# Performance work log

Hardware: AMD Instinct MI355X
Metric: run time of the kernel (lower is better)

The kernel has to match this reference:

```python
import jax, jax.numpy as jnp
import numpy as np

HEADS = 16
TOPK = 2048  # dsa_topk


def setup_inputs() -> dict:
    key = jax.random.key(0)
    ks = jax.random.split(key, 9)
    B, Q, KV, C = 2, 2048, 16384, 1024
    w = lambda k: jax.random.normal(k, (C, C), dtype=jnp.float32) * 0.02
    return {
        "hidden_states": jax.random.normal(ks[0], (B, Q, C), dtype=jnp.float32),
        "encoder_hidden_states": jax.random.normal(ks[1], (B, KV, C), dtype=jnp.float32),
        "Wq": w(ks[2]),
        "Wk": w(ks[3]),
        "Wv": w(ks[4]),
        "Wo": w(ks[5]),
        "bo": jnp.zeros((C,), dtype=jnp.float32),
        "Wg": jax.random.normal(ks[6], (C, C), dtype=jnp.float32) * 0.01,  # xavier gain 0.1
        "bg": jnp.full((C,), -1.5, dtype=jnp.float32),  # gate_init_bias
    }


def reference(hidden_states, encoder_hidden_states, Wq, Wk, Wv, Wo, bo, Wg, bg):
    B, Q, C = hidden_states.shape
    H = HEADS
    D = C // H
    scale = 1.0 / jnp.sqrt(jnp.asarray(D, dtype=hidden_states.dtype))

    # projections -> [B, H, S, D]
    q = (hidden_states @ Wq).reshape(B, Q, H, D).transpose(0, 2, 1, 3)
    k = (encoder_hidden_states @ Wk).reshape(B, -1, H, D).transpose(0, 2, 1, 3)
    v = (encoder_hidden_states @ Wv).reshape(B, -1, H, D).transpose(0, 2, 1, 3)

    # _sparse_select: query-summary scored top-k KV gather (kv_len > TOPK here)
    q_summary = q.mean(axis=2)                                   # [B, H, D]
    sel_score = jnp.einsum("bhd,bhkd->bhk", q_summary, k) * scale
    idx = jax.lax.top_k(sel_score, TOPK)[1]                      # [B, H, TOPK]
    k_sel = jnp.take_along_axis(k, idx[..., None], axis=2)       # [B, H, TOPK, D]
    v_sel = jnp.take_along_axis(v, idx[..., None], axis=2)

    # attention over selected KV
    scores = jnp.einsum("bhqd,bhkd->bhqk", q, k_sel) * scale
    probs = jax.nn.softmax(scores.astype(jnp.float32), axis=-1).astype(scores.dtype)
    out = jnp.einsum("bhqk,bhkd->bhqd", probs, v_sel)
    out = out.transpose(0, 2, 1, 3).reshape(B, Q, C)

    # sigmoid gate + output projection (to_out[1] dropout is identity at eval)
    out = out * jax.nn.sigmoid(out @ Wg + bg)
    out = out @ Wo + bo

    # residual_connection=True, rescale_output_factor=1.0
    return out + hidden_states
```

## Files before the change

kernel.cpp:

```cpp
#include <hip/hip_runtime.h>
#include <hip/hip_bf16.h>

typedef unsigned short u16;
typedef __bf16 bf16x8 __attribute__((ext_vector_type(8)));
typedef float f32x4 __attribute__((ext_vector_type(4)));

__device__ __forceinline__ u16 f2bf(float f) {
    union { float f; unsigned int u; } v; v.f = f;
    unsigned int u = v.u;
    unsigned int r = (u + 0x7fffu + ((u >> 16) & 1u)) >> 16;
    return (u16)r;
}
__device__ __forceinline__ float bf2f(u16 b) {
    union { unsigned int u; float f; } v; v.u = ((unsigned int)b) << 16;
    return v.f;
}

__device__ __forceinline__ void glds16(const u16* g, u16* l) {
    __builtin_amdgcn_global_load_lds(
        (__attribute__((address_space(1))) void*)(g),
        (__attribute__((address_space(3))) void*)(l), 16, 0, 0);
}

__global__ __launch_bounds__(256) void cast_bf16_kernel(const float* __restrict__ src,
                                                        u16* __restrict__ dst, int n4) {
    int i = blockIdx.x * 256 + threadIdx.x;
    if (i >= n4) return;
    float4 v = ((const float4*)src)[i];
    ushort4 o;
    o.x = f2bf(v.x); o.y = f2bf(v.y); o.z = f2bf(v.z); o.w = f2bf(v.w);
    ((ushort4*)dst)[i] = o;
}

__global__ __launch_bounds__(256) void transpose_cast_kernel(
    const float* __restrict__ Wq, const float* __restrict__ Wk, const float* __restrict__ Wv,
    const float* __restrict__ Wg, const float* __restrict__ Wo,
    u16* __restrict__ WqT, u16* __restrict__ WkvT, u16* __restrict__ WgT, u16* __restrict__ WoT) {
    __shared__ float tile[32][33];
    const float* src; u16* dst;
    switch (blockIdx.z) {
        case 0: src = Wq; dst = WqT; break;
        case 1: src = Wk; dst = WkvT; break;
        case 2: src = Wv; dst = WkvT + (size_t)1024 * 1024; break;
        case 3: src = Wg; dst = WgT; break;
        default: src = Wo; dst = WoT; break;
    }
    int n0 = blockIdx.x * 32, k0 = blockIdx.y * 32;
    int tx = threadIdx.x, ty = threadIdx.y;
    #pragma unroll
    for (int j = 0; j < 4; j++)
        tile[ty + j * 8][tx] = src[(size_t)(k0 + ty + j * 8) * 1024 + n0 + tx];
    __syncthreads();
    #pragma unroll
    for (int j = 0; j < 4; j++)
        dst[(size_t)(n0 + ty + j * 8) * 1024 + k0 + tx] = f2bf(tile[tx][ty + j * 8]);
}

template <int EPI>
__global__ __launch_bounds__(256) void gemm_bf16(
    const u16* __restrict__ A, const u16* __restrict__ B, int ldc,
    u16* __restrict__ Cbf, const float* __restrict__ bias,
    const u16* __restrict__ mul_src, const float* __restrict__ add_src,
    float* __restrict__ Cf) {
    constexpr int K = 1024;
    const int tid = threadIdx.x;
    const int w = tid >> 6, l = tid & 63;
    const int lr = l & 15, lg = l >> 4;
    const int wr = w >> 1, wc = w & 1;
    const int m0 = blockIdx.y * 128, n0 = blockIdx.x * 128;

    __shared__ u16 As[128 * 64];
    __shared__ u16 Bs[128 * 64];

    const f32x4 fz = {0.f, 0.f, 0.f, 0.f};
    f32x4 acc[4][4];
    #pragma unroll
    for (int i = 0; i < 4; i++)
        #pragma unroll
        for (int j = 0; j < 4; j++) acc[i][j] = fz;

    const int lane_row = l >> 3;
    const int lane_sl  = l & 7;
    const int src_ch   = lane_sl ^ lane_row;
    const u16* Ab = A + (size_t)(m0 + w * 32 + lane_row) * K + src_ch * 8;
    const u16* Bb = B + (size_t)(n0 + w * 32 + lane_row) * K + src_ch * 8;

    for (int kt = 0; kt < K; kt += 64) {
        __syncthreads();
        #pragma unroll
        for (int j = 0; j < 4; j++) {
            glds16(Ab + (size_t)j * 8 * K + kt, As + (w * 32 + j * 8) * 64);
            glds16(Bb + (size_t)j * 8 * K + kt, Bs + (w * 32 + j * 8) * 64);
        }
        __syncthreads();
        #pragma unroll
        for (int kk = 0; kk < 2; kk++) {
            bf16x8 af[4], bfr[4];
            #pragma unroll
            for (int mi = 0; mi < 4; mi++) {
                int row = wr * 64 + mi * 16 + lr;
                int ch = (kk * 4 + lg) ^ (row & 7);
                af[mi] = *(const bf16x8*)(As + row * 64 + ch * 8);
            }
            #pragma unroll
            for (int ni = 0; ni < 4; ni++) {
                int row = wc * 64 + ni * 16 + lr;
                int ch = (kk * 4 + lg) ^ (row & 7);
                bfr[ni] = *(const bf16x8*)(Bs + row * 64 + ch * 8);
            }
            #pragma unroll
            for (int mi = 0; mi < 4; mi++)
                #pragma unroll
                for (int ni = 0; ni < 4; ni++)
                    acc[mi][ni] = __builtin_amdgcn_mfma_f32_16x16x32_bf16(
                        af[mi], bfr[ni], acc[mi][ni], 0, 0, 0);
        }
    }

    #pragma unroll
    for (int mi = 0; mi < 4; mi++) {
        #pragma unroll
        for (int ni = 0; ni < 4; ni++) {
            #pragma unroll
            for (int r = 0; r < 4; r++) {
                int gm = m0 + wr * 64 + mi * 16 + lg * 4 + r;
                int gn = n0 + wc * 64 + ni * 16 + lr;
                float v = acc[mi][ni][r];
                if (EPI == 0) {
                    Cbf[(size_t)gm * ldc + gn] = f2bf(v);
                } else if (EPI == 2) {
                    float g = v + bias[gn];
                    float a = bf2f(mul_src[(size_t)gm * ldc + gn]);
                    float sg = 1.f / (1.f + __expf(-g));
                    Cbf[(size_t)gm * ldc + gn] = f2bf(a * sg);
                } else {
                    Cf[(size_t)gm * ldc + gn] = v + bias[gn] + add_src[(size_t)gm * ldc + gn];
                }
            }
        }
    }
}

__global__ __launch_bounds__(256) void hsum1_kernel(const float* __restrict__ hidden,
                                                    float* __restrict__ part) {
    int b = blockIdx.x, chunk = blockIdx.y;
    int tid = threadIdx.x;
    const float4* src = (const float4*)(hidden + ((size_t)b * 2048 + chunk * 16) * 1024) + tid;
    float4 acc = {0.f, 0.f, 0.f, 0.f};
    #pragma unroll
    for (int r = 0; r < 16; r++) {
        float4 v = src[r * 256];
        acc.x += v.x; acc.y += v.y; acc.z += v.z; acc.w += v.w;
    }
    ((float4*)(part + ((size_t)b * 128 + chunk) * 1024))[tid] = acc;
}

__global__ __launch_bounds__(256) void hsum2_kernel(const float* __restrict__ part,
                                                    float* __restrict__ hm) {
    int b = blockIdx.x, tid = threadIdx.x;
    const float4* src = (const float4*)(part + (size_t)b * 128 * 1024) + tid;
    float4 acc = {0.f, 0.f, 0.f, 0.f};
    for (int c = 0; c < 128; c++) {
        float4 v = src[c * 256];
        acc.x += v.x; acc.y += v.y; acc.z += v.z; acc.w += v.w;
    }
    const float inv = 1.f / 2048.f;
    acc.x *= inv; acc.y *= inv; acc.z *= inv; acc.w *= inv;
    ((float4*)(hm + (size_t)b * 1024))[tid] = acc;
}

__global__ __launch_bounds__(256) void qz_kernel(const float* __restrict__ hm,
                                                 const u16* __restrict__ WqT,
                                                 const u16* __restrict__ WkT,
                                                 u16* __restrict__ z_bf) {
    int bh = blockIdx.x, b = bh >> 4, h = bh & 15;
    int tid = threadIdx.x;
    __shared__ float hm_l[1024];
    __shared__ float qs_l[64];
    __shared__ float red[256];
    ((float4*)hm_l)[tid] = ((const float4*)(hm + (size_t)b * 1024))[tid];
    __syncthreads();
    {
        int d = tid >> 2, q = tid & 3;
        const u16* wq = WqT + (size_t)(h * 64 + d) * 1024 + q * 256;
        float a = 0.f;
        for (int i = 0; i < 256; i += 8) {
            uint4 u = *(const uint4*)(wq + i);
            const u16* p = (const u16*)&u;
            #pragma unroll
            for (int j = 0; j < 8; j++) a += bf2f(p[j]) * hm_l[q * 256 + i + j];
        }
        red[tid] = a;
    }
    __syncthreads();
    if (tid < 64)
        qs_l[tid] = red[tid * 4] + red[tid * 4 + 1] + red[tid * 4 + 2] + red[tid * 4 + 3];
    __syncthreads();
    {
        float z0 = 0.f, z1 = 0.f, z2 = 0.f, z3 = 0.f;
        for (int d = 0; d < 64; d++) {
            float qs = qs_l[d];
            const u16* wk = WkT + (size_t)(h * 64 + d) * 1024 + tid * 4;
            uint2 u = *(const uint2*)wk;
            const u16* p = (const u16*)&u;
            z0 += qs * bf2f(p[0]); z1 += qs * bf2f(p[1]);
            z2 += qs * bf2f(p[2]); z3 += qs * bf2f(p[3]);
        }
        ushort4 o;
        o.x = f2bf(z0); o.y = f2bf(z1); o.z = f2bf(z2); o.w = f2bf(z3);
        *(ushort4*)(z_bf + (size_t)bh * 1024 + tid * 4) = o;
    }
}

__global__ __launch_bounds__(256) void escore_kernel(const float* __restrict__ enc,
                                                     const u16* __restrict__ z_bf,
                                                     u16* __restrict__ ebf,
                                                     float* __restrict__ score) {
    const int b = blockIdx.y, kv0 = blockIdx.x * 64;
    const int tid = threadIdx.x, w = tid >> 6, l = tid & 63;
    const int lr = l & 15, lg = l >> 4;
    __shared__ u16 e_lds[64 * 64];

    const int row2 = tid >> 3;
    const int cgrp = tid & 7;
    const float* ebase = enc + (size_t)(b * 16384 + kv0) * 1024;
    u16* obase = ebf + (size_t)(b * 16384 + kv0) * 1024;
    const u16* zb = z_bf + (size_t)b * 16 * 1024;

    float4 rv[2][2];
    auto loadT = [&](int kt) {
        #pragma unroll
        for (int jj = 0; jj < 2; jj++) {
            int row = row2 + jj * 32;
            rv[jj][0] = *(const float4*)(ebase + (size_t)row * 1024 + kt + cgrp * 8);
            rv[jj][1] = *(const float4*)(ebase + (size_t)row * 1024 + kt + cgrp * 8 + 4);
        }
    };
    loadT(0);

    const f32x4 fz = {0.f, 0.f, 0.f, 0.f};
    f32x4 acc = fz;

    for (int kt = 0; kt < 1024; kt += 64) {
        #pragma unroll
        for (int jj = 0; jj < 2; jj++) {
            int row = row2 + jj * 32;
            union { u16 u[8]; uint4 v; } pk;
            pk.u[0] = f2bf(rv[jj][0].x); pk.u[1] = f2bf(rv[jj][0].y);
            pk.u[2] = f2bf(rv[jj][0].z); pk.u[3] = f2bf(rv[jj][0].w);
            pk.u[4] = f2bf(rv[jj][1].x); pk.u[5] = f2bf(rv[jj][1].y);
            pk.u[6] = f2bf(rv[jj][1].z); pk.u[7] = f2bf(rv[jj][1].w);
            *(uint4*)(e_lds + row * 64 + ((cgrp ^ (row & 7)) * 8)) = pk.v;
            *(uint4*)(obase + (size_t)row * 1024 + kt + cgrp * 8) = pk.v;
        }
        __syncthreads();
        if (kt + 64 < 1024) loadT(kt + 64);
        #pragma unroll
        for (int ks = 0; ks < 2; ks++) {
            bf16x8 af = *(const bf16x8*)(zb + (size_t)lr * 1024 + kt + ks * 32 + lg * 8);
            int brow = w * 16 + lr;
            bf16x8 bf_ = *(const bf16x8*)(e_lds + brow * 64 + (((ks * 4 + lg) ^ (brow & 7))) * 8);
            acc = __builtin_amdgcn_mfma_f32_16x16x32_bf16(af, bf_, acc, 0, 0, 0);
        }
        __syncthreads();
    }
    #pragma unroll
    for (int r = 0; r < 4; r++)
        score[(size_t)(b * 16 + lg * 4 + r) * 16384 + kv0 + w * 16 + lr] = acc[r];
}

__global__ __launch_bounds__(1024) void select_kernel(const float* __restrict__ score,
                                                      int* __restrict__ sel_idx) {
    const int bh = blockIdx.x;
    const float* sc = score + (size_t)bh * 16384;
    const int tid = threadIdx.x;
    const int grp = tid >> 8;

    __shared__ int hist[4][256];
    __shared__ int total[256];
    __shared__ int bc[4];

    u16 key[16];
    #pragma unroll
    for (int j = 0; j < 16; j++) {
        unsigned int b = __float_as_uint(sc[tid + j * 1024]);
        unsigned int ui = (b & 0x80000000u) ? ~b : (b | 0x80000000u);
        key[j] = (u16)(ui >> 16);
    }

    ((int*)hist)[tid] = 0;
    __syncthreads();
    #pragma unroll
    for (int j = 0; j < 16; j++) atomicAdd(&hist[grp][key[j] >> 8], 1);
    __syncthreads();
    if (tid < 256) total[tid] = hist[0][tid] + hist[1][tid] + hist[2][tid] + hist[3][tid];
    __syncthreads();
    if (tid == 0) {
        int want = 2048, acc = 0;
        for (int dd = 255; dd >= 0; dd--) {
            acc += total[dd];
            if (acc >= want) { bc[0] = dd; bc[1] = want - (acc - total[dd]); break; }
        }
    }
    __syncthreads();
    const int hi = bc[0];
    const int want1 = bc[1];

    ((int*)hist)[tid] = 0;
    __syncthreads();
    #pragma unroll
    for (int j = 0; j < 16; j++)
        if ((key[j] >> 8) == hi) atomicAdd(&hist[grp][key[j] & 0xff], 1);
    __syncthreads();
    if (tid < 256) total[tid] = hist[0][tid] + hist[1][tid] + hist[2][tid] + hist[3][tid];
    __syncthreads();
    if (tid == 0) {
        int want = want1, acc = 0;
        for (int dd = 255; dd >= 0; dd--) {
            acc += total[dd];
            if (acc >= want) { bc[0] = (hi << 8) | dd; bc[1] = want - (acc - total[dd]); break; }
        }
        bc[2] = 0; bc[3] = 0;
    }
    __syncthreads();
    const u16 thr = (u16)bc[0];
    const int n_eq = bc[1];
    const int base_eq = 2048 - n_eq;

    int* out = sel_idx + (size_t)bh * 2048;
    #pragma unroll
    for (int j = 0; j < 16; j++) {
        int i = tid + j * 1024;
        if (key[j] > thr) {
            int p = atomicAdd(&bc[2], 1);
            out[p] = i;
        } else if (key[j] == thr) {
            int p = atomicAdd(&bc[3], 1);
            if (p < n_eq) out[base_eq + p] = i;
        }
    }
}

__global__ __launch_bounds__(256) void selproj_kernel(const u16* __restrict__ ebf,
                                                      const u16* __restrict__ WkvT,
                                                      const int* __restrict__ sel_idx,
                                                      u16* __restrict__ k_sel,
                                                      u16* __restrict__ v_selT) {
    const int bh = blockIdx.y, b = bh >> 4, h = bh & 15;
    const int t0 = blockIdx.x * 128;
    const int tid = threadIdx.x, w = tid >> 6, l = tid & 63;
    const int lr = l & 15, lg = l >> 4;
    const int lane_row = l >> 3, src_ch = (l & 7) ^ lane_row;

    __shared__ u16 e_lds[128 * 64];
    __shared__ u16 w_lds[128 * 64];

    int encrow[4], wrow[4];
    #pragma unroll
    for (int j = 0; j < 4; j++) {
        int t = t0 + w * 32 + j * 8 + lane_row;
        encrow[j] = b * 16384 + sel_idx[(size_t)bh * 2048 + t];
        int r = w * 32 + j * 8 + lane_row;
        wrow[j] = (r < 64) ? (h * 64 + r) : (1024 + h * 64 + (r & 63));
    }

    const f32x4 fz = {0.f, 0.f, 0.f, 0.f};
    f32x4 acc_k[2][4], acc_v[8];
    #pragma unroll
    for (int i = 0; i < 2; i++)
        #pragma unroll
        for (int j = 0; j < 4; j++) acc_k[i][j] = fz;
    #pragma unroll
    for (int i = 0; i < 8; i++) acc_v[i] = fz;

    for (int kt = 0; kt < 1024; kt += 64) {
        __syncthreads();
        #pragma unroll
        for (int j = 0; j < 4; j++) {
            glds16(ebf + (size_t)encrow[j] * 1024 + kt + src_ch * 8, e_lds + (w * 32 + j * 8) * 64);
            glds16(WkvT + (size_t)wrow[j] * 1024 + kt + src_ch * 8, w_lds + (w * 32 + j * 8) * 64);
        }
        __syncthreads();
        #pragma unroll
        for (int ks = 0; ks < 2; ks++) {
            bf16x8 ae[2];
            #pragma unroll
            for (int mi = 0; mi < 2; mi++) {
                int row = w * 32 + mi * 16 + lr;
                ae[mi] = *(const bf16x8*)(e_lds + row * 64 + (((ks * 4 + lg) ^ (row & 7))) * 8);
            }
            bf16x8 aw;
            {
                int row = 64 + w * 16 + lr;
                aw = *(const bf16x8*)(w_lds + row * 64 + (((ks * 4 + lg) ^ (row & 7))) * 8);
            }
            #pragma unroll
            for (int ni = 0; ni < 4; ni++) {
                int row = ni * 16 + lr;
                bf16x8 bw = *(const bf16x8*)(w_lds + row * 64 + (((ks * 4 + lg) ^ (row & 7))) * 8);
                acc_k[0][ni] = __builtin_amdgcn_mfma_f32_16x16x32_bf16(ae[0], bw, acc_k[0][ni], 0, 0, 0);
                acc_k[1][ni] = __builtin_amdgcn_mfma_f32_16x16x32_bf16(ae[1], bw, acc_k[1][ni], 0, 0, 0);
            }
            #pragma unroll
            for (int ni = 0; ni < 8; ni++) {
                int row = ni * 16 + lr;
                bf16x8 be = *(const bf16x8*)(e_lds + row * 64 + (((ks * 4 + lg) ^ (row & 7))) * 8);
                acc_v[ni] = __builtin_amdgcn_mfma_f32_16x16x32_bf16(aw, be, acc_v[ni], 0, 0, 0);
            }
        }
    }

    u16* kb = k_sel + (size_t)bh * 2048 * 64;
    #pragma unroll
    for (int mi = 0; mi < 2; mi++)
        #pragma unroll
        for (int ni = 0; ni < 4; ni++)
            #pragma unroll
            for (int r = 0; r < 4; r++) {
                int t = t0 + w * 32 + mi * 16 + lg * 4 + r;
                int d = ni * 16 + lr;
                kb[(size_t)t * 64 + (((d >> 3) ^ (t & 7)) * 8) + (d & 7)] = f2bf(acc_k[mi][ni][r]);
            }
    u16* vb = v_selT + (size_t)bh * 64 * 2048;
    #pragma unroll
    for (int ni = 0; ni < 8; ni++)
        #pragma unroll
        for (int r = 0; r < 4; r++) {
            int d = w * 16 + lg * 4 + r;
            int t = t0 + ni * 16 + lr;
            int tl = t & 63;
            int kap = (tl & 15) * 4 + (tl >> 4);
            vb[(size_t)d * 2048 + (t & ~63) + (((kap >> 3) ^ (d & 7)) * 8) + (kap & 7)] =
                f2bf(acc_v[ni][r]);
        }
}

__global__ __launch_bounds__(512) void attn_kernel(
    const u16* __restrict__ q_bf, const u16* __restrict__ k_sel,
    const u16* __restrict__ v_selT, u16* __restrict__ attn_out) {
    const int bh = blockIdx.y, b = bh >> 4, h = bh & 15;
    const int q0 = blockIdx.x * 128;
    const int tid = threadIdx.x, w = tid >> 6, l = tid & 63;
    const int lr = l & 15, lg = l >> 4;
    const int lk = lr & 7;
    const float SC = 0.18033688011f;
    const float THR = 11.0f;

    __shared__ u16 k_lds[2][64 * 64];
    __shared__ u16 vt_lds[64 * 64];
    __shared__ u16 p_lds[8][16][68];

    const u16* qb = q_bf + ((size_t)b * 2048 + q0 + w * 16 + lr) * 1024 + h * 64;
    bf16x8 qf0 = *(const bf16x8*)(qb + lg * 8);
    bf16x8 qf1 = *(const bf16x8*)(qb + 32 + lg * 8);

    const f32x4 fz = {0.f, 0.f, 0.f, 0.f};
    f32x4 o[4];
    #pragma unroll
    for (int f = 0; f < 4; f++) o[f] = fz;
    float mm = -1e30f;
    float l_part[4] = {0.f, 0.f, 0.f, 0.f};

    const u16* kb  = k_sel + (size_t)bh * 2048 * 64;
    const u16* vtb = v_selT + (size_t)bh * 64 * 2048;

    auto stageK = [&](int it, int buf) {
        const u16* ksrc = kb + (size_t)(it * 64 + w * 8) * 64 + (size_t)l * 8;
        glds16(ksrc, k_lds[buf] + (w * 8) * 64);
    };
    auto stageV = [&](int it) {
        const u16* vsrc = vtb + (size_t)(w * 8 + (l >> 3)) * 2048 + it * 64 + (l & 7) * 8;
        glds16(vsrc, vt_lds + (w * 8) * 64);
    };

    stageK(0, 0);
    __syncthreads();

    #pragma unroll 1
    for (int it = 0; it < 32; ++it) {
        const int cur = it & 1;
        stageV(it);
        if (it + 1 < 32) stageK(it + 1, cur ^ 1);

        f32x4 s[4];
        #pragma unroll
        for (int c = 0; c < 4; c++) s[c] = fz;
        __builtin_amdgcn_s_setprio(1);
        #pragma unroll
        for (int c = 0; c < 4; c++) {
            const u16* krow = k_lds[cur] + (c * 16 + lr) * 64;
            bf16x8 kf0 = *(const bf16x8*)(krow + (lg ^ lk) * 8);
            s[c] = __builtin_amdgcn_mfma_f32_16x16x32_bf16(qf0, kf0, s[c], 0, 0, 0);
            bf16x8 kf1 = *(const bf16x8*)(krow + (((4 + lg) ^ lk)) * 8);
            s[c] = __builtin_amdgcn_mfma_f32_16x16x32_bf16(qf1, kf1, s[c], 0, 0, 0);
        }
        __builtin_amdgcn_s_setprio(0);

        float mx = s[0][0];
        #pragma unroll
        for (int c = 0; c < 4; c++)
            #pragma unroll
            for (int r = 0; r < 4; r++) mx = fmaxf(mx, s[c][r]);
        mx = fmaxf(mx, __shfl_xor(mx, 1));
        mx = fmaxf(mx, __shfl_xor(mx, 2));
        mx = fmaxf(mx, __shfl_xor(mx, 4));
        mx = fmaxf(mx, __shfl_xor(mx, 8));
        mx = fmaxf(mx, __shfl_xor(mx, 16));
        mx = fmaxf(mx, __shfl_xor(mx, 32));
        mx *= SC;
        if (mx > mm + THR) {
            float al = __builtin_amdgcn_exp2f(mm - mx);
            mm = mx;
            #pragma unroll
            for (int r = 0; r < 4; r++) l_part[r] *= al;
            #pragma unroll
            for (int f = 0; f < 4; f++)
                #pragma unroll
                for (int r = 0; r < 4; r++) o[f][r] *= al;
        }
        #pragma unroll
        for (int r = 0; r < 4; r++) {
            ushort4 pk;
            u16 pb[4];
            #pragma unroll
            for (int c = 0; c < 4; c++) {
                float p = __builtin_amdgcn_exp2f(__builtin_fmaf(s[c][r], SC, -mm));
                l_part[r] += p;
                __bf16 hv = (__bf16)p;
                pb[c] = *(u16*)&hv;
            }
            pk.x = pb[0]; pk.y = pb[1]; pk.z = pb[2]; pk.w = pb[3];
            *(ushort4*)(&p_lds[w][lg * 4 + r][lr * 4]) = pk;
        }

        if (it + 1 < 32) {
            asm volatile("s_waitcnt vmcnt(1)" ::: "memory");
        } else {
            asm volatile("s_waitcnt vmcnt(0)" ::: "memory");
        }
        __builtin_amdgcn_sched_barrier(0);
        __builtin_amdgcn_s_barrier();

        __builtin_amdgcn_s_setprio(1);
        #pragma unroll
        for (int kk = 0; kk < 2; kk++) {
            bf16x8 ap = *(const bf16x8*)(&p_lds[w][lr][kk * 32 + lg * 8]);
            #pragma unroll
            for (int f = 0; f < 4; f++) {
                const u16* vrow = vt_lds + (f * 16 + lr) * 64;
                bf16x8 bv = *(const bf16x8*)(vrow + (((kk * 4 + lg) ^ lk)) * 8);
                o[f] = __builtin_amdgcn_mfma_f32_16x16x32_bf16(ap, bv, o[f], 0, 0, 0);
            }
        }
        __builtin_amdgcn_s_setprio(0);

        __syncthreads();
    }

    float invl[4];
    #pragma unroll
    for (int r = 0; r < 4; r++) {
        float lr_ = l_part[r];
        lr_ += __shfl_xor(lr_, 1);
        lr_ += __shfl_xor(lr_, 2);
        lr_ += __shfl_xor(lr_, 4);
        lr_ += __shfl_xor(lr_, 8);
        invl[r] = 1.f / lr_;
    }
    u16* ob = attn_out + ((size_t)b * 2048 + q0 + w * 16 + lg * 4) * 1024 + h * 64 + lr;
    #pragma unroll
    for (int f = 0; f < 4; f++) {
        #pragma unroll
        for (int r = 0; r < 4; r++) {
            __bf16 hv = (__bf16)(o[f][r] * invl[r]);
            ob[(size_t)r * 1024 + f * 16] = *(u16*)&hv;
        }
    }
}

extern "C" void kernel_launch(void* const* d_in, const int* in_sizes, int n_in,
                              void* d_out, int out_size, void* d_ws, size_t ws_size,
                              hipStream_t stream) {
    const float* hidden = (const float*)d_in[0];
    const float* enc    = (const float*)d_in[1];
    const float* Wq = (const float*)d_in[2];
    const float* Wk = (const float*)d_in[3];
    const float* Wv = (const float*)d_in[4];
    const float* Wo = (const float*)d_in[5];
    const float* bo = (const float*)d_in[6];
    const float* Wg = (const float*)d_in[7];
    const float* bg = (const float*)d_in[8];
    float* out = (float*)d_out;

    char* ws = (char*)d_ws;
    size_t off = 0;
    auto alloc = [&](size_t bytes) -> char* {
        char* p = ws + off;
        off += (bytes + 255) & ~(size_t)255;
        return p;
    };
    u16* hbf   = (u16*)alloc(4096ull * 1024 * 2);
    u16* ebf   = (u16*)alloc(32768ull * 1024 * 2);
    u16* WqT   = (u16*)alloc(1024ull * 1024 * 2);
    u16* WkvT  = (u16*)alloc(2048ull * 1024 * 2);
    u16* WgT   = (u16*)alloc(1024ull * 1024 * 2);
    u16* WoT   = (u16*)alloc(1024ull * 1024 * 2);
    u16* q_bf  = (u16*)alloc(4096ull * 1024 * 2);
    float* hm  = (float*)alloc(2ull * 1024 * 4);
    float* part = (float*)alloc(2ull * 128 * 1024 * 4);
    u16* z_bf  = (u16*)alloc(32ull * 1024 * 2);
    float* scor = (float*)alloc(32ull * 16384 * 4);
    int* sel    = (int*)alloc(32ull * 2048 * 4);
    u16* ksel   = (u16*)alloc(32ull * 2048 * 64 * 2);
    u16* vT     = (u16*)alloc(32ull * 64 * 2048 * 2);
    u16* attn   = (u16*)alloc(4096ull * 1024 * 2);
    u16* gate   = (u16*)alloc(4096ull * 1024 * 2);
    (void)ws_size; (void)in_sizes; (void)n_in; (void)out_size;

    hsum1_kernel<<<dim3(2, 128), 256, 0, stream>>>(hidden, part);
    hsum2_kernel<<<2, 256, 0, stream>>>(part, hm);
    cast_bf16_kernel<<<4096, 256, 0, stream>>>(hidden, hbf, 1048576);
    transpose_cast_kernel<<<dim3(32, 32, 5), dim3(32, 8), 0, stream>>>(
        Wq, Wk, Wv, Wg, Wo, WqT, WkvT, WgT, WoT);

    qz_kernel<<<32, 256, 0, stream>>>(hm, WqT, WkvT, z_bf);
    escore_kernel<<<dim3(256, 2), 256, 0, stream>>>(enc, z_bf, ebf, scor);
    select_kernel<<<32, 1024, 0, stream>>>(scor, sel);
    selproj_kernel<<<dim3(16, 32), 256, 0, stream>>>(ebf, WkvT, sel, ksel, vT);

    gemm_bf16<0><<<dim3(8, 32), 256, 0, stream>>>(hbf, WqT, 1024, q_bf, nullptr, nullptr, nullptr, nullptr);
    attn_kernel<<<dim3(16, 32), 512, 0, stream>>>(q_bf, ksel, vT, attn);

    gemm_bf16<2><<<dim3(8, 32), 256, 0, stream>>>(attn, WgT, 1024, gate, bg, attn, nullptr, nullptr);
    gemm_bf16<3><<<dim3(8, 32), 256, 0, stream>>>(gate, WoT, 1024, nullptr, bo, nullptr, hidden, out);
}
```

Baseline: 252.2 us.

## Split encoder cast from scoring and double-buffer LDS staging in score/selproj

Moves the fp32-to-bf16 cast of encoder states out of the scoring kernel into a standalone cast kernel. The scoring kernel then streams bf16 rows into double-buffered LDS through direct global-to-LDS loads with per-wave vmcnt waits instead of block barriers. The selected-KV projection kernel also gains double-buffered LDS staging, so the next tile's loads overlap the current tile's MFMAs, and raises wave priority around the MFMA block. The cost is that the bf16 encoder tensor is written and then read back in full, which adds a large amount of memory traffic.

```diff
diff --git a/kernel.cpp b/kernel.cpp
--- a/kernel.cpp
+++ b/kernel.cpp
@@ -212,57 +212,47 @@
     }
 }
 
-__global__ __launch_bounds__(256) void escore_kernel(const float* __restrict__ enc,
-                                                     const u16* __restrict__ z_bf,
-                                                     u16* __restrict__ ebf,
-                                                     float* __restrict__ score) {
+__global__ __launch_bounds__(256) void score_kernel(const u16* __restrict__ ebf,
+                                                    const u16* __restrict__ z_bf,
+                                                    float* __restrict__ score) {
     const int b = blockIdx.y, kv0 = blockIdx.x * 64;
     const int tid = threadIdx.x, w = tid >> 6, l = tid & 63;
     const int lr = l & 15, lg = l >> 4;
-    __shared__ u16 e_lds[64 * 64];
-
-    const int row2 = tid >> 3;
-    const int cgrp = tid & 7;
-    const float* ebase = enc + (size_t)(b * 16384 + kv0) * 1024;
-    u16* obase = ebf + (size_t)(b * 16384 + kv0) * 1024;
+    __shared__ u16 e_lds[2][64 * 64];
+
+    const u16* eb = ebf + (size_t)(b * 16384 + kv0) * 1024;
     const u16* zb = z_bf + (size_t)b * 16 * 1024;
-
-    float4 rv[2][2];
-    auto loadT = [&](int kt) {
-        #pragma unroll
-        for (int jj = 0; jj < 2; jj++) {
-            int row = row2 + jj * 32;
-            rv[jj][0] = *(const float4*)(ebase + (size_t)row * 1024 + kt + cgrp * 8);
-            rv[jj][1] = *(const float4*)(ebase + (size_t)row * 1024 + kt + cgrp * 8 + 4);
-        }
+    const int lrow = l >> 3, lch = l & 7;
+    const int src_ch = lch ^ lrow;
+
+    auto stage = [&](int kt, int buf) {
+        const u16* s0 = eb + (size_t)(w * 16 + lrow) * 1024 + kt + src_ch * 8;
+        glds16(s0,            e_lds[buf] + (w * 16) * 64);
+        glds16(s0 + 8 * 1024, e_lds[buf] + (w * 16 + 8) * 64);
     };
-    loadT(0);
+    stage(0, 0);
 
     const f32x4 fz = {0.f, 0.f, 0.f, 0.f};
     f32x4 acc = fz;
 
-    for (int kt = 0; kt < 1024; kt += 64) {
-        #pragma unroll
-        for (int jj = 0; jj < 2; jj++) {
-            int row = row2 + jj * 32;
-            union { u16 u[8]; uint4 v; } pk;
-            pk.u[0] = f2bf(rv[jj][0].x); pk.u[1] = f2bf(rv[jj][0].y);
-            pk.u[2] = f2bf(rv[jj][0].z); pk.u[3] = f2bf(rv[jj][0].w);
-            pk.u[4] = f2bf(rv[jj][1].x); pk.u[5] = f2bf(rv[jj][1].y);
-            pk.u[6] = f2bf(rv[jj][1].z); pk.u[7] = f2bf(rv[jj][1].w);
-            *(uint4*)(e_lds + row * 64 + ((cgrp ^ (row & 7)) * 8)) = pk.v;
-            *(uint4*)(obase + (size_t)row * 1024 + kt + cgrp * 8) = pk.v;
-        }
-        __syncthreads();
-        if (kt + 64 < 1024) loadT(kt + 64);
+    #pragma unroll 1
+    for (int t = 0; t < 16; ++t) {
+        const int kt = t * 64;
+        if (t + 1 < 16) {
+            stage(kt + 64, (t & 1) ^ 1);
+            asm volatile("s_waitcnt vmcnt(2)" ::: "memory");
+        } else {
+            asm volatile("s_waitcnt vmcnt(0)" ::: "memory");
+        }
+        __builtin_amdgcn_sched_barrier(0);
+        const u16* ecur = e_lds[t & 1];
         #pragma unroll
         for (int ks = 0; ks < 2; ks++) {
             bf16x8 af = *(const bf16x8*)(zb + (size_t)lr * 1024 + kt + ks * 32 + lg * 8);
-            int brow = w * 16 + lr;
-            bf16x8 bf_ = *(const bf16x8*)(e_lds + brow * 64 + (((ks * 4 + lg) ^ (brow & 7))) * 8);
+            int row = w * 16 + lr;
+            bf16x8 bf_ = *(const bf16x8*)(ecur + row * 64 + (((ks * 4 + lg) ^ (row & 7))) * 8);
             acc = __builtin_amdgcn_mfma_f32_16x16x32_bf16(af, bf_, acc, 0, 0, 0);
         }
-        __syncthreads();
     }
     #pragma unroll
     for (int r = 0; r < 4; r++)
@@ -352,8 +342,8 @@
     const int lr = l & 15, lg = l >> 4;
     const int lane_row = l >> 3, src_ch = (l & 7) ^ lane_row;
 
-    __shared__ u16 e_lds[128 * 64];
-    __shared__ u16 w_lds[128 * 64];
+    __shared__ u16 e_lds[2][128 * 64];
+    __shared__ u16 w_lds[2][128 * 64];
 
     int encrow[4], wrow[4];
     #pragma unroll
@@ -364,6 +354,16 @@
         wrow[j] = (r < 64) ? (h * 64 + r) : (1024 + h * 64 + (r & 63));
     }
 
+    auto stage = [&](int kt, int buf) {
+        #pragma unroll
+        for (int j = 0; j < 4; j++) {
+            glds16(ebf + (size_t)encrow[j] * 1024 + kt + src_ch * 8,
+                   e_lds[buf] + (w * 32 + j * 8) * 64);
+            glds16(WkvT + (size_t)wrow[j] * 1024 + kt + src_ch * 8,
+                   w_lds[buf] + (w * 32 + j * 8) * 64);
+        }
+    };
+
     const f32x4 fz = {0.f, 0.f, 0.f, 0.f};
     f32x4 acc_k[2][4], acc_v[8];
     #pragma unroll
@@ -373,41 +373,47 @@
     #pragma unroll
     for (int i = 0; i < 8; i++) acc_v[i] = fz;
 
-    for (int kt = 0; kt < 1024; kt += 64) {
-        __syncthreads();
-        #pragma unroll
-        for (int j = 0; j < 4; j++) {
-            glds16(ebf + (size_t)encrow[j] * 1024 + kt + src_ch * 8, e_lds + (w * 32 + j * 8) * 64);
-            glds16(WkvT + (size_t)wrow[j] * 1024 + kt + src_ch * 8, w_lds + (w * 32 + j * 8) * 64);
-        }
-        __syncthreads();
+    stage(0, 0);
+    __syncthreads();
+
+    #pragma unroll 1
+    for (int t = 0; t < 16; ++t) {
+        const int kt = t * 64;
+        const int cur = t & 1;
+        if (t + 1 < 16) stage(kt + 64, cur ^ 1);
+
+        const u16* ec = e_lds[cur];
+        const u16* wc_ = w_lds[cur];
+        __builtin_amdgcn_s_setprio(1);
         #pragma unroll
         for (int ks = 0; ks < 2; ks++) {
             bf16x8 ae[2];
             #pragma unroll
             for (int mi = 0; mi < 2; mi++) {
                 int row = w * 32 + mi * 16 + lr;
-                ae[mi] = *(const bf16x8*)(e_lds + row * 64 + (((ks * 4 + lg) ^ (row & 7))) * 8);
+                ae[mi] = *(const bf16x8*)(ec + row * 64 + (((ks * 4 + lg) ^ (row & 7))) * 8);
             }
             bf16x8 aw;
             {
                 int row = 64 + w * 16 + lr;
-                aw = *(const bf16x8*)(w_lds + row * 64 + (((ks * 4 + lg) ^ (row & 7))) * 8);
+                aw = *(const bf16x8*)(wc_ + row * 64 + (((ks * 4 + lg) ^ (row & 7))) * 8);
             }
             #pragma unroll
             for (int ni = 0; ni < 4; ni++) {
                 int row = ni * 16 + lr;
-                bf16x8 bw = *(const bf16x8*)(w_lds + row * 64 + (((ks * 4 + lg) ^ (row & 7))) * 8);
+                bf16x8 bw = *(const bf16x8*)(wc_ + row * 64 + (((ks * 4 + lg) ^ (row & 7))) * 8);
                 acc_k[0][ni] = __builtin_amdgcn_mfma_f32_16x16x32_bf16(ae[0], bw, acc_k[0][ni], 0, 0, 0);
                 acc_k[1][ni] = __builtin_amdgcn_mfma_f32_16x16x32_bf16(ae[1], bw, acc_k[1][ni], 0, 0, 0);
             }
             #pragma unroll
             for (int ni = 0; ni < 8; ni++) {
                 int row = ni * 16 + lr;
-                bf16x8 be = *(const bf16x8*)(e_lds + row * 64 + (((ks * 4 + lg) ^ (row & 7))) * 8);
+                bf16x8 be = *(const bf16x8*)(ec + row * 64 + (((ks * 4 + lg) ^ (row & 7))) * 8);
                 acc_v[ni] = __builtin_amdgcn_mfma_f32_16x16x32_bf16(aw, be, acc_v[ni], 0, 0, 0);
             }
         }
+        __builtin_amdgcn_s_setprio(0);
+        __syncthreads();
     }
 
     u16* kb = k_sel + (size_t)bh * 2048 * 64;
@@ -620,11 +626,12 @@
     hsum1_kernel<<<dim3(2, 128), 256, 0, stream>>>(hidden, part);
     hsum2_kernel<<<2, 256, 0, stream>>>(part, hm);
     cast_bf16_kernel<<<4096, 256, 0, stream>>>(hidden, hbf, 1048576);
+    cast_bf16_kernel<<<32768, 256, 0, stream>>>(enc, ebf, 8388608);
     transpose_cast_kernel<<<dim3(32, 32, 5), dim3(32, 8), 0, stream>>>(
         Wq, Wk, Wv, Wg, Wo, WqT, WkvT, WgT, WoT);
 
     qz_kernel<<<32, 256, 0, stream>>>(hm, WqT, WkvT, z_bf);
-    escore_kernel<<<dim3(256, 2), 256, 0, stream>>>(enc, z_bf, ebf, scor);
+    score_kernel<<<dim3(256, 2), 256, 0, stream>>>(ebf, z_bf, scor);
     select_kernel<<<32, 1024, 0, stream>>>(scor, sel);
     selproj_kernel<<<dim3(16, 32), 256, 0, stream>>>(ebf, WkvT, sel, ksel, vT);
 
```

Measured after the change: 253.0 us. No clear change (+0.3%).
